# Optimization experiments

Hardware: AMD Instinct MI355X
Metric: run time of the kernel (lower is better)

## Reference

```python
import jax, jax.numpy as jnp
import numpy as np

NUM_CHANNELS = 512
B_DIM = 64
C_DIM = 16
N = 512
FEAT = NUM_CHANNELS * 4 * 4  # 8192


def setup_inputs() -> dict:
    key = jax.random.key(0)
    k1, k2 = jax.random.split(key)
    inp = jax.random.normal(k1, (N, NUM_CHANNELS, 4, 4), dtype=jnp.float32)
    T = jax.random.normal(k2, (FEAT, B_DIM * C_DIM), dtype=jnp.float32) * 0.1
    return {"inp": inp, "T": T}


def reference(inp, T):
    x = inp.reshape(-1, FEAT)                      # (N, 8192)
    M = (x @ T).reshape(-1, B_DIM, C_DIM)          # (N, B, C)
    # pairwise L1 distance over C: (N, N, B)
    dist = jnp.sum(jnp.abs(M[:, None, :, :] - M[None, :, :, :]), axis=-1)
    o = jnp.sum(jnp.exp(-dist), axis=1)            # (N, B)
    return jnp.concatenate((x, o), axis=1)         # (N, 8192 + B)
```

## Files before the change

kernel.cpp:

```cpp
#include <hip/hip_runtime.h>

#define NROWS 512
#define FEAT  8192
#define BDIM  64
#define CDIM  16
#define MCOLS 1024
#define OUTC  8256
#define KSPLIT 8
#define KCHUNK (FEAT / KSPLIT)
#define MSIZE  (NROWS * MCOLS)

typedef __bf16 bf16x8 __attribute__((ext_vector_type(8)));
typedef float  floatx4 __attribute__((ext_vector_type(4)));

#define AS1 __attribute__((address_space(1)))
#define AS3 __attribute__((address_space(3)))

static __device__ __forceinline__ void gload16(const void* g, void* l) {
    __builtin_amdgcn_global_load_lds((AS1 void*)(g), (AS3 void*)(l), 16, 0, 0);
}

static __device__ __forceinline__ unsigned short f2bf(float f) {
    unsigned int x = __builtin_bit_cast(unsigned int, f);
    unsigned int r = (x + 0x7FFFu + ((x >> 16) & 1u)) >> 16;
    return (unsigned short)r;
}

__global__ __launch_bounds__(512, 2) void k_prep(const float* __restrict__ x,
                                                 const float* __restrict__ T,
                                                 unsigned short* __restrict__ xb,
                                                 unsigned short* __restrict__ Tt,
                                                 float* __restrict__ out) {
    __shared__ __align__(16) float lds[2][64][65];
    int bid = blockIdx.x, t = threadIdx.x;
#pragma unroll
    for (int u = 0; u < 8; ++u) {
        int gid = bid * 4096 + u * 512 + t;
        float4 v = *(const float4*)(x + (size_t)gid * 4);
        ushort4 uu;
        uu.x = f2bf(v.x); uu.y = f2bf(v.y); uu.z = f2bf(v.z); uu.w = f2bf(v.w);
        *(ushort4*)(xb + (size_t)gid * 4) = uu;
        int row = gid >> 11, col4 = gid & 2047;
        *(float4*)(out + (size_t)row * OUTC + col4 * 4) = v;
    }
    int sub = t >> 8, tt = t & 255;
    for (int u = 0; u < 4; ++u) {
        int tile = bid * 8 + u * 2 + sub;
        int kt = tile & 127, nt = tile >> 7;
        __syncthreads();
        int kk = tt >> 2, q = tt & 3;
#pragma unroll
        for (int p = 0; p < 4; ++p) {
            int c4 = q + p * 4;
            float4 v = *(const float4*)(T + (size_t)(kt * 64 + kk) * MCOLS + nt * 64 + c4 * 4);
            lds[sub][kk][c4 * 4 + 0] = v.x; lds[sub][kk][c4 * 4 + 1] = v.y;
            lds[sub][kk][c4 * 4 + 2] = v.z; lds[sub][kk][c4 * 4 + 3] = v.w;
        }
        __syncthreads();
        int nr = tt >> 2, ck = tt & 3;
        unsigned int wv[8];
#pragma unroll
        for (int j = 0; j < 8; ++j) {
            unsigned int lo = f2bf(lds[sub][ck * 16 + j * 2 + 0][nr]);
            unsigned int hi = f2bf(lds[sub][ck * 16 + j * 2 + 1][nr]);
            wv[j] = lo | (hi << 16);
        }
        uint4* dst = (uint4*)(Tt + (size_t)(nt * 64 + nr) * FEAT + kt * 64 + ck * 16);
        dst[0] = make_uint4(wv[0], wv[1], wv[2], wv[3]);
        dst[1] = make_uint4(wv[4], wv[5], wv[6], wv[7]);
    }
}

__global__ __launch_bounds__(512, 2) void k_gemm(const unsigned short* __restrict__ xb,
                                                 const unsigned short* __restrict__ Tt,
                                                 float* __restrict__ Mp) {
    __shared__ __align__(16) unsigned short ldsA[128 * 32];
    __shared__ __align__(16) unsigned short ldsB[128 * 32];
    int bid = blockIdx.x, t = threadIdx.x;
    int mt = bid & 3, nt = (bid >> 2) & 7, ks = bid >> 5;
    int m0 = mt * 128, n0 = nt * 128, kbase = ks * KCHUNK;
    int w = t >> 6, l = t & 63;

    int r0 = w * 16 + (l >> 2);
    int c  = (l & 3) ^ ((r0 >> 1) & 3);
    const unsigned short* gA = xb + (size_t)(m0 + r0) * FEAT + kbase + c * 8;
    const unsigned short* gB = Tt + (size_t)(n0 + r0) * FEAT + kbase + c * 8;
    unsigned short* lA = ldsA + w * 512;
    unsigned short* lB = ldsB + w * 512;

    int wr = w >> 2, wc = w & 3, fm = l & 15, fq = l >> 4;
    int swz = (fm >> 1) & 3;
    const unsigned short* pa[4];
    const unsigned short* pb[2];
#pragma unroll
    for (int a = 0; a < 4; ++a)
        pa[a] = ldsA + (wr * 64 + a * 16 + fm) * 32 + ((fq ^ swz) * 8);
#pragma unroll
    for (int b = 0; b < 2; ++b)
        pb[b] = ldsB + (wc * 32 + b * 16 + fm) * 32 + ((fq ^ swz) * 8);

    floatx4 acc[4][2] = {};

    for (int kk = 0; kk < KCHUNK; kk += 32) {
        __syncthreads();
        gload16(gA + kk, lA);
        gload16(gB + kk, lB);
        __syncthreads();
        bf16x8 af[4], bfr[2];
#pragma unroll
        for (int a = 0; a < 4; ++a) af[a] = *(const bf16x8*)pa[a];
#pragma unroll
        for (int b = 0; b < 2; ++b) bfr[b] = *(const bf16x8*)pb[b];
#pragma unroll
        for (int a = 0; a < 4; ++a)
#pragma unroll
            for (int b = 0; b < 2; ++b)
                acc[a][b] = __builtin_amdgcn_mfma_f32_16x16x32_bf16(af[a], bfr[b], acc[a][b], 0, 0, 0);
    }

    float* outp = Mp + (size_t)ks * MSIZE;
    int gr0 = m0 + wr * 64, gc0 = n0 + wc * 32;
#pragma unroll
    for (int a = 0; a < 4; ++a)
#pragma unroll
        for (int r = 0; r < 4; ++r) {
            int row = gr0 + a * 16 + fq * 4 + r;
#pragma unroll
            for (int b = 0; b < 2; ++b)
                outp[(size_t)row * MCOLS + gc0 + b * 16 + fm] = acc[a][b][r];
        }
}

__global__ __launch_bounds__(512, 2) void k_pair(const float* __restrict__ Mp,
                                                 float* __restrict__ out) {
    __shared__ float ldsM[NROWS * 20];
    __shared__ float partial[8][64];
    int bid = blockIdx.x, t = threadIdx.x;
    int b = bid & 63, itp = bid >> 6;
#pragma unroll
    for (int p = 0; p < 4; ++p) {
        int idx = t + p * 512;
        int j = idx >> 2, c4 = idx & 3;
        const float* base = Mp + (size_t)j * MCOLS + b * CDIM + c4 * 4;
        float4 s = *(const float4*)base;
#pragma unroll
        for (int k = 1; k < KSPLIT; ++k) {
            float4 v = *(const float4*)(base + (size_t)k * MSIZE);
            s.x += v.x; s.y += v.y; s.z += v.z; s.w += v.w;
        }
        *(float4*)&ldsM[j * 20 + c4 * 4] = s;
    }
    __syncthreads();

    int lane = t & 63, w = t >> 6, g = t >> 8, wg = (t >> 6) & 3;
    int i = (itp * 2 + g) * 64 + lane;
    float mi[CDIM];
#pragma unroll
    for (int cc = 0; cc < CDIM; ++cc) mi[cc] = ldsM[i * 20 + cc];

    float acc = 0.0f;
    for (int jj = wg * 128; jj < wg * 128 + 128; ++jj) {
        float d = 0.0f;
#pragma unroll
        for (int cc = 0; cc < CDIM; ++cc) d += fabsf(mi[cc] - ldsM[jj * 20 + cc]);
        acc += __expf(-d);
    }
    partial[w][lane] = acc;
    __syncthreads();
    if ((t & 255) < 64) {
        int ii = (itp * 2 + g) * 64 + (t & 63);
        float o = partial[g * 4 + 0][t & 63] + partial[g * 4 + 1][t & 63] +
                  partial[g * 4 + 2][t & 63] + partial[g * 4 + 3][t & 63];
        out[(size_t)ii * OUTC + FEAT + b] = o;
    }
}

extern "C" void kernel_launch(void* const* d_in, const int* in_sizes, int n_in,
                              void* d_out, int out_size, void* d_ws, size_t ws_size,
                              hipStream_t stream) {
    const float* x = (const float*)d_in[0];
    const float* T = (const float*)d_in[1];
    float* out = (float*)d_out;

    unsigned short* xb = (unsigned short*)d_ws;
    unsigned short* Tt = (unsigned short*)((char*)d_ws + (8u << 20));
    float*          Mp = (float*)((char*)d_ws + (24u << 20));

    k_prep<<<256, 512, 0, stream>>>(x, T, xb, Tt, out);
    k_gemm<<<256, 512, 0, stream>>>(xb, Tt, Mp);
    k_pair<<<256, 512, 0, stream>>>(Mp, out);
}
```

Baseline: 138.8 us.

## Retile GEMM to 128x64 tiles with 64-wide K steps and 4 waves

The split-K GEMM moves from 128x128 output tiles with 8 waves and K-step 32 to 128x64 tiles with 4 waves and K-step 64. Grid size doubles to 512 blocks of 256 threads, and each thread issues six async global-to-LDS loads per iteration. Each iteration now runs two MFMA half-steps, which halves the number of barrier pairs per K chunk. The cost is more total global reads of the A operand, because A is reloaded for twice as many N tiles.

```diff
diff --git a/kernel.cpp b/kernel.cpp
--- a/kernel.cpp
+++ b/kernel.cpp
@@ -71,51 +71,57 @@
     }
 }
 
-__global__ __launch_bounds__(512, 2) void k_gemm(const unsigned short* __restrict__ xb,
+__global__ __launch_bounds__(256, 2) void k_gemm(const unsigned short* __restrict__ xb,
                                                  const unsigned short* __restrict__ Tt,
                                                  float* __restrict__ Mp) {
-    __shared__ __align__(16) unsigned short ldsA[128 * 32];
-    __shared__ __align__(16) unsigned short ldsB[128 * 32];
+    __shared__ __align__(16) unsigned short ldsA[128 * 64];
+    __shared__ __align__(16) unsigned short ldsB[64 * 64];
     int bid = blockIdx.x, t = threadIdx.x;
-    int mt = bid & 3, nt = (bid >> 2) & 7, ks = bid >> 5;
-    int m0 = mt * 128, n0 = nt * 128, kbase = ks * KCHUNK;
+    int mt = bid & 3, nt = (bid >> 2) & 15, ks = bid >> 6;
+    int m0 = mt * 128, n0 = nt * 64, kbase = ks * KCHUNK;
     int w = t >> 6, l = t & 63;
 
-    int r0 = w * 16 + (l >> 2);
-    int c  = (l & 3) ^ ((r0 >> 1) & 3);
-    const unsigned short* gA = xb + (size_t)(m0 + r0) * FEAT + kbase + c * 8;
-    const unsigned short* gB = Tt + (size_t)(n0 + r0) * FEAT + kbase + c * 8;
-    unsigned short* lA = ldsA + w * 512;
-    unsigned short* lB = ldsB + w * 512;
+    int c  = (l & 3) ^ ((l >> 3) & 3);
+    int lr = l >> 2;
+    const unsigned short* gA0 = xb + (size_t)(m0 + w * 32 + lr) * FEAT + kbase + c * 8;
+    const unsigned short* gA1 = gA0 + (size_t)16 * FEAT;
+    const unsigned short* gB0 = Tt + (size_t)(n0 + w * 16 + lr) * FEAT + kbase + c * 8;
+    unsigned short* lA00 = ldsA + (4 * w + 0) * 512;
+    unsigned short* lA01 = ldsA + (4 * w + 1) * 512;
+    unsigned short* lA10 = ldsA + (4 * w + 2) * 512;
+    unsigned short* lA11 = ldsA + (4 * w + 3) * 512;
+    unsigned short* lB0  = ldsB + (2 * w + 0) * 512;
+    unsigned short* lB1  = ldsB + (2 * w + 1) * 512;
 
-    int wr = w >> 2, wc = w & 3, fm = l & 15, fq = l >> 4;
-    int swz = (fm >> 1) & 3;
-    const unsigned short* pa[4];
-    const unsigned short* pb[2];
-#pragma unroll
-    for (int a = 0; a < 4; ++a)
-        pa[a] = ldsA + (wr * 64 + a * 16 + fm) * 32 + ((fq ^ swz) * 8);
-#pragma unroll
-    for (int b = 0; b < 2; ++b)
-        pb[b] = ldsB + (wc * 32 + b * 16 + fm) * 32 + ((fq ^ swz) * 8);
+    int wr = w >> 1, wc = w & 1, fm = l & 15, fq = l >> 4;
+    int fo = fm * 32 + ((fq ^ ((fm >> 1) & 3)) * 8);
+    const unsigned short* paB = ldsA + (wr * 8) * 512 + fo;
+    const unsigned short* pbB = ldsB + (wc * 4) * 512 + fo;
 
     floatx4 acc[4][2] = {};
 
-    for (int kk = 0; kk < KCHUNK; kk += 32) {
+    for (int kk = 0; kk < KCHUNK; kk += 64) {
         __syncthreads();
-        gload16(gA + kk, lA);
-        gload16(gB + kk, lB);
+        gload16(gA0 + kk,      lA00);
+        gload16(gA0 + kk + 32, lA01);
+        gload16(gA1 + kk,      lA10);
+        gload16(gA1 + kk + 32, lA11);
+        gload16(gB0 + kk,      lB0);
+        gload16(gB0 + kk + 32, lB1);
         __syncthreads();
-        bf16x8 af[4], bfr[2];
 #pragma unroll
-        for (int a = 0; a < 4; ++a) af[a] = *(const bf16x8*)pa[a];
+        for (int h = 0; h < 2; ++h) {
+            bf16x8 af[4], bfr[2];
 #pragma unroll
-        for (int b = 0; b < 2; ++b) bfr[b] = *(const bf16x8*)pb[b];
+            for (int a = 0; a < 4; ++a) af[a]  = *(const bf16x8*)(paB + (a * 2 + h) * 512);
 #pragma unroll
-        for (int a = 0; a < 4; ++a)
+            for (int b = 0; b < 2; ++b) bfr[b] = *(const bf16x8*)(pbB + (b * 2 + h) * 512);
 #pragma unroll
-            for (int b = 0; b < 2; ++b)
-                acc[a][b] = __builtin_amdgcn_mfma_f32_16x16x32_bf16(af[a], bfr[b], acc[a][b], 0, 0, 0);
+            for (int a = 0; a < 4; ++a)
+#pragma unroll
+                for (int b = 0; b < 2; ++b)
+                    acc[a][b] = __builtin_amdgcn_mfma_f32_16x16x32_bf16(af[a], bfr[b], acc[a][b], 0, 0, 0);
+        }
     }
 
     float* outp = Mp + (size_t)ks * MSIZE;
@@ -187,6 +193,6 @@
     float*          Mp = (float*)((char*)d_ws + (24u << 20));
 
     k_prep<<<256, 512, 0, stream>>>(x, T, xb, Tt, out);
-    k_gemm<<<256, 512, 0, stream>>>(xb, Tt, Mp);
+    k_gemm<<<512, 256, 0, stream>>>(xb, Tt, Mp);
     k_pair<<<256, 512, 0, stream>>>(Mp, out);
 }
```

Measured after the change: 136.0 us, median of 2. 2.0% less time.
